# Optimization experiments

Hardware: AMD Instinct MI355X
Metric: run time of the kernel (lower is better)

The kernel has to match this reference:

```python
import jax, jax.numpy as jnp
import numpy as np

MAX_REL = 8  # max_relative_position
B, H, L, D = 2, 16, 2048, 64


def setup_inputs() -> dict:
    key = jax.random.key(0)
    kq, kk, kv, kb = jax.random.split(key, 4)
    return {
        "q": jax.random.normal(kq, (B, H, L, D), dtype=jnp.float32),
        "k": jax.random.normal(kk, (B, H, L, D), dtype=jnp.float32),
        "v": jax.random.normal(kv, (B, H, L, D), dtype=jnp.float32),
        "relative_bias": jax.random.normal(kb, (2 * MAX_REL + 1,), dtype=jnp.float32),
    }


def reference(q, k, v, relative_bias):
    Bq, Hq, Lq, Dq = q.shape
    scale = jnp.sqrt(jnp.asarray(Dq, dtype=q.dtype))
    # [B,H,L,L] attention scores
    scores = jnp.einsum("bhqd,bhkd->bhqk", q, k) / scale
    pos = jnp.arange(Lq)
    rel = pos[None, :] - pos[:, None]                 # [L,L] (col - row), matches torch code
    idx = jnp.clip(rel, -MAX_REL, MAX_REL) + MAX_REL  # [L,L] in [0, 2*MAX_REL]
    bias = relative_bias[idx]                         # [L,L] gather from bias table
    scores = scores + bias[None, None, :, :]
    attn = jax.nn.softmax(scores, axis=-1)
    return jnp.einsum("bhqk,bhkd->bhqd", attn, v)
```

## Files before the change

### kernel.cpp

```cpp
#include <hip/hip_runtime.h>
#include <hip/hip_bf16.h>


#define LOG2E 1.44269504088896f

constexpr int Lv = 2048, Dv = 64;
constexpr int BH  = 32;
constexpr int BQ  = 128;
constexpr int WQ  = 32;
constexpr int BKT = 64;
constexpr int NQT = Lv / BQ;
constexpr int NKT = Lv / BKT;
constexpr int LDK = 72;
constexpr int MAXREL = 8;

typedef __bf16 bf16x8 __attribute__((ext_vector_type(8)));
typedef __bf16 bf16x4 __attribute__((ext_vector_type(4)));
typedef float  f32x4  __attribute__((ext_vector_type(4)));

static __device__ __forceinline__ unsigned pack2bf(float a, float b) {
    __bf16 x = (__bf16)a, y = (__bf16)b;
    unsigned short ux = __builtin_bit_cast(unsigned short, x);
    unsigned short uy = __builtin_bit_cast(unsigned short, y);
    return (unsigned)ux | ((unsigned)uy << 16);
}

__global__ __launch_bounds__(256, 2) void relattn_kernel(
    const float* __restrict__ Q, const float* __restrict__ K,
    const float* __restrict__ V, const float* __restrict__ RB,
    float* __restrict__ O)
{
    __shared__ __align__(16) __bf16 sK[2][BKT * LDK];
    __shared__ __align__(16) __bf16 sV[2][Dv * LDK];
    __shared__ float sRB[2 * MAXREL + 1];

    const int tid  = threadIdx.x;
    const int w    = tid >> 6;
    const int lane = tid & 63;
    const int l16  = lane & 15;
    const int lg   = lane >> 4;

    const int bh = blockIdx.x & (BH - 1);
    const int qt = blockIdx.x >> 5;

    const size_t base = (size_t)bh * Lv * Dv;
    const float* Qb = Q + base + (size_t)qt * BQ * Dv;
    const float* Kb = K + base;
    const float* Vb = V + base;
    float*       Ob = O + base + (size_t)qt * BQ * Dv;

    if (tid < 2 * MAXREL + 1) sRB[tid] = RB[tid] * LOG2E;

    const float qsc = 0.125f * LOG2E;
    bf16x8 qfrag[2][2];
    #pragma unroll
    for (int h = 0; h < 2; ++h) {
        const float* qrow = Qb + (w * WQ + h * 16 + l16) * Dv;
        #pragma unroll
        for (int s = 0; s < 2; ++s) {
            const float4 a = *(const float4*)(qrow + lg * 8 + 32 * s);
            const float4 b = *(const float4*)(qrow + lg * 8 + 32 * s + 4);
            bf16x8 f;
            f[0] = (__bf16)(a.x * qsc); f[1] = (__bf16)(a.y * qsc);
            f[2] = (__bf16)(a.z * qsc); f[3] = (__bf16)(a.w * qsc);
            f[4] = (__bf16)(b.x * qsc); f[5] = (__bf16)(b.y * qsc);
            f[6] = (__bf16)(b.z * qsc); f[7] = (__bf16)(b.w * qsc);
            qfrag[h][s] = f;
        }
    }

    f32x4 oacc[2][4];
    f32x4 lacc[2];
    #pragma unroll
    for (int h = 0; h < 2; ++h) {
        lacc[h] = (f32x4){0.f, 0.f, 0.f, 0.f};
        #pragma unroll
        for (int t = 0; t < 4; ++t)
            #pragma unroll
            for (int r = 0; r < 4; ++r) oacc[h][t][r] = 0.f;
    }

    const int kr0 = tid >> 4;
    const int kc4 = (tid & 15) * 4;
    const int vkk0 = (tid & 31) * 2;
    const int vd0  = (tid >> 5) * 8;
    const int vcol = (vkk0 & 35) | ((vkk0 & 12) << 1) | ((vkk0 & 16) >> 2);

    float4 kreg[4], vreg[4];
    auto loadKV = [&](int kt) {
        const float* Ks = Kb + (size_t)kt * BKT * Dv;
        const float* Vs = Vb + (size_t)kt * BKT * Dv;
        #pragma unroll
        for (int p = 0; p < 4; ++p)
            kreg[p] = *(const float4*)(Ks + (p * 16 + kr0) * Dv + kc4);
        vreg[0] = *(const float4*)(Vs + vkk0 * Dv + vd0);
        vreg[1] = *(const float4*)(Vs + vkk0 * Dv + vd0 + 4);
        vreg[2] = *(const float4*)(Vs + (vkk0 + 1) * Dv + vd0);
        vreg[3] = *(const float4*)(Vs + (vkk0 + 1) * Dv + vd0 + 4);
    };

    loadKV(0);

    const int qw0 = qt * BQ + w * WQ;
    const int qgl = qw0 + l16;

    for (int kt = 0; kt < NKT; ++kt) {
        const int buf = kt & 1;
        #pragma unroll
        for (int p = 0; p < 4; ++p) {
            bf16x4 pk;
            pk[0] = (__bf16)kreg[p].x; pk[1] = (__bf16)kreg[p].y;
            pk[2] = (__bf16)kreg[p].z; pk[3] = (__bf16)kreg[p].w;
            *(bf16x4*)&sK[buf][(p * 16 + kr0) * LDK + kc4] = pk;
        }
        #pragma unroll
        for (int j = 0; j < 4; ++j) {
            *(unsigned*)&sV[buf][(vd0 + j) * LDK + vcol] =
                pack2bf(vreg[0][j], vreg[2][j]);
            *(unsigned*)&sV[buf][(vd0 + 4 + j) * LDK + vcol] =
                pack2bf(vreg[1][j], vreg[3][j]);
        }
        __syncthreads();

        if (kt + 1 < NKT) loadKV(kt + 1);

        f32x4 sacc[2][4];
        #pragma unroll
        for (int h = 0; h < 2; ++h)
            #pragma unroll
            for (int t = 0; t < 4; ++t)
                #pragma unroll
                for (int r = 0; r < 4; ++r) sacc[h][t][r] = 0.f;
        #pragma unroll
        for (int s = 0; s < 2; ++s) {
            #pragma unroll
            for (int t = 0; t < 4; ++t) {
                bf16x8 a = *(const bf16x8*)&sK[buf][(t * 16 + l16) * LDK + lg * 8 + 32 * s];
                sacc[0][t] = __builtin_amdgcn_mfma_f32_16x16x32_bf16(a, qfrag[0][s], sacc[0][t], 0, 0, 0);
                sacc[1][t] = __builtin_amdgcn_mfma_f32_16x16x32_bf16(a, qfrag[1][s], sacc[1][t], 0, 0, 0);
            }
        }

        const int k0 = kt * BKT;
        bf16x8 pfrag[2][2];
        #pragma unroll
        for (int h = 0; h < 2; ++h) {
            const int qw0h = qw0 + h * 16;
            if (k0 >= qw0h + 15 + MAXREL) {
                const float bc = sRB[2 * MAXREL];
                #pragma unroll
                for (int t = 0; t < 4; ++t)
                    #pragma unroll
                    for (int r = 0; r < 4; ++r) {
                        float p = __builtin_amdgcn_exp2f(sacc[h][t][r] + bc);
                        lacc[h][r] += p;
                        pfrag[h][t >> 1][(t & 1) * 4 + r] = (__bf16)p;
                    }
            } else if (k0 + BKT - 1 + MAXREL <= qw0h) {
                const float bc = sRB[0];
                #pragma unroll
                for (int t = 0; t < 4; ++t)
                    #pragma unroll
                    for (int r = 0; r < 4; ++r) {
                        float p = __builtin_amdgcn_exp2f(sacc[h][t][r] + bc);
                        lacc[h][r] += p;
                        pfrag[h][t >> 1][(t & 1) * 4 + r] = (__bf16)p;
                    }
            } else {
                const int kkb = k0 + lg * 4 - (qgl + h * 16);
                #pragma unroll
                for (int t = 0; t < 4; ++t) {
                    #pragma unroll
                    for (int r = 0; r < 4; ++r) {
                        int d = kkb + t * 16 + r;
                        d = d < -MAXREL ? -MAXREL : (d > MAXREL ? MAXREL : d);
                        float p = __builtin_amdgcn_exp2f(sacc[h][t][r] + sRB[d + MAXREL]);
                        lacc[h][r] += p;
                        pfrag[h][t >> 1][(t & 1) * 4 + r] = (__bf16)p;
                    }
                }
            }
        }

        #pragma unroll
        for (int s = 0; s < 2; ++s) {
            #pragma unroll
            for (int t = 0; t < 4; ++t) {
                bf16x8 vf = *(const bf16x8*)&sV[buf][(t * 16 + l16) * LDK + lg * 8 + 32 * s];
                oacc[0][t] = __builtin_amdgcn_mfma_f32_16x16x32_bf16(vf, pfrag[0][s], oacc[0][t], 0, 0, 0);
                oacc[1][t] = __builtin_amdgcn_mfma_f32_16x16x32_bf16(vf, pfrag[1][s], oacc[1][t], 0, 0, 0);
            }
        }
    }

    #pragma unroll
    for (int h = 0; h < 2; ++h) {
        float l = lacc[h][0] + lacc[h][1] + lacc[h][2] + lacc[h][3];
        l += __shfl_xor(l, 16);
        l += __shfl_xor(l, 32);
        const float linv = 1.f / l;
        float* orow = Ob + (w * WQ + h * 16 + l16) * Dv;
        #pragma unroll
        for (int t = 0; t < 4; ++t) {
            float4 o;
            o.x = oacc[h][t][0] * linv; o.y = oacc[h][t][1] * linv;
            o.z = oacc[h][t][2] * linv; o.w = oacc[h][t][3] * linv;
            *(float4*)(orow + t * 16 + lg * 4) = o;
        }
    }
}

extern "C" void kernel_launch(void* const* d_in, const int* in_sizes, int n_in,
                              void* d_out, int out_size, void* d_ws, size_t ws_size,
                              hipStream_t stream) {
    const float* q  = (const float*)d_in[0];
    const float* k  = (const float*)d_in[1];
    const float* v  = (const float*)d_in[2];
    const float* rb = (const float*)d_in[3];
    float* out = (float*)d_out;
    relattn_kernel<<<dim3(BH * NQT), dim3(256), 0, stream>>>(q, k, v, rb, out);
}
```

Baseline: 136.9 us.

## Split key range across two blocks and combine partial outputs in a second kernel

The kernel is templated on a key-split count. With two splits, each block handles half of the key tiles and writes its unnormalized output accumulator and row sum to workspace. A new combine kernel adds the two partials and normalizes. Launch bounds are raised to four blocks per CU, so the doubled grid can fill the device with more concurrent waves. In exchange it writes and re-reads partial results, adds a second launch, tightens the register budget, which risks spills, and only runs when the workspace is large enough.

```diff
diff --git a/kernel.cpp b/kernel.cpp
--- a/kernel.cpp
+++ b/kernel.cpp
@@ -7,7 +7,6 @@
 constexpr int Lv = 2048, Dv = 64;
 constexpr int BH  = 32;
 constexpr int BQ  = 128;
-constexpr int WQ  = 32;
 constexpr int BKT = 64;
 constexpr int NQT = Lv / BQ;
 constexpr int NKT = Lv / BKT;
@@ -25,11 +24,15 @@
     return (unsigned)ux | ((unsigned)uy << 16);
 }
 
-__global__ __launch_bounds__(256, 2) void relattn_kernel(
+template<int NSPLIT>
+__global__ __launch_bounds__(256, 4) void relattn_kernel(
     const float* __restrict__ Q, const float* __restrict__ K,
     const float* __restrict__ V, const float* __restrict__ RB,
-    float* __restrict__ O)
+    float* __restrict__ Out, float* __restrict__ Opart,
+    float* __restrict__ Lpart)
 {
+    constexpr int NI = NKT / NSPLIT;
+
     __shared__ __align__(16) __bf16 sK[2][BKT * LDK];
     __shared__ __align__(16) __bf16 sV[2][Dv * LDK];
     __shared__ float sRB[2 * MAXREL + 1];
@@ -40,14 +43,15 @@
     const int l16  = lane & 15;
     const int lg   = lane >> 4;
 
-    const int bh = blockIdx.x & (BH - 1);
-    const int qt = blockIdx.x >> 5;
+    const int bid = blockIdx.x;
+    const int bh  = bid & (BH - 1);
+    const int qt  = (bid >> 5) & (NQT - 1);
+    const int sp  = bid >> 9;
 
     const size_t base = (size_t)bh * Lv * Dv;
     const float* Qb = Q + base + (size_t)qt * BQ * Dv;
     const float* Kb = K + base;
     const float* Vb = V + base;
-    float*       Ob = O + base + (size_t)qt * BQ * Dv;
 
     if (tid < 2 * MAXREL + 1) sRB[tid] = RB[tid] * LOG2E;
 
@@ -55,7 +59,7 @@
     bf16x8 qfrag[2][2];
     #pragma unroll
     for (int h = 0; h < 2; ++h) {
-        const float* qrow = Qb + (w * WQ + h * 16 + l16) * Dv;
+        const float* qrow = Qb + (w * 32 + h * 16 + l16) * Dv;
         #pragma unroll
         for (int s = 0; s < 2; ++s) {
             const float4 a = *(const float4*)(qrow + lg * 8 + 32 * s);
@@ -99,13 +103,15 @@
         vreg[3] = *(const float4*)(Vs + (vkk0 + 1) * Dv + vd0 + 4);
     };
 
-    loadKV(0);
-
-    const int qw0 = qt * BQ + w * WQ;
+    const int kt0 = sp * NI;
+    loadKV(kt0);
+
+    const int qw0 = qt * BQ + w * 32;
     const int qgl = qw0 + l16;
 
-    for (int kt = 0; kt < NKT; ++kt) {
-        const int buf = kt & 1;
+    for (int i = 0; i < NI; ++i) {
+        const int buf = i & 1;
+        const int kt  = kt0 + i;
         #pragma unroll
         for (int p = 0; p < 4; ++p) {
             bf16x4 pk;
@@ -122,7 +128,7 @@
         }
         __syncthreads();
 
-        if (kt + 1 < NKT) loadKV(kt + 1);
+        if (i + 1 < NI) loadKV(kt + 1);
 
         f32x4 sacc[2][4];
         #pragma unroll
@@ -198,16 +204,41 @@
         float l = lacc[h][0] + lacc[h][1] + lacc[h][2] + lacc[h][3];
         l += __shfl_xor(l, 16);
         l += __shfl_xor(l, 32);
-        const float linv = 1.f / l;
-        float* orow = Ob + (w * WQ + h * 16 + l16) * Dv;
-        #pragma unroll
-        for (int t = 0; t < 4; ++t) {
-            float4 o;
-            o.x = oacc[h][t][0] * linv; o.y = oacc[h][t][1] * linv;
-            o.z = oacc[h][t][2] * linv; o.w = oacc[h][t][3] * linv;
-            *(float4*)(orow + t * 16 + lg * 4) = o;
-        }
-    }
+        const int q = w * 32 + h * 16 + l16;
+        if (NSPLIT == 1) {
+            const float linv = 1.f / l;
+            float* orow = Out + base + (size_t)(qt * BQ + q) * Dv;
+            #pragma unroll
+            for (int t = 0; t < 4; ++t) {
+                float4 o;
+                o.x = oacc[h][t][0] * linv; o.y = oacc[h][t][1] * linv;
+                o.z = oacc[h][t][2] * linv; o.w = oacc[h][t][3] * linv;
+                *(float4*)(orow + t * 16 + lg * 4) = o;
+            }
+        } else {
+            const size_t prow = (size_t)(sp * BH + bh) * Lv + qt * BQ + q;
+            if (lg == 0) Lpart[prow] = l;
+            float* orow = Opart + prow * Dv;
+            #pragma unroll
+            for (int t = 0; t < 4; ++t)
+                *(f32x4*)(orow + t * 16 + lg * 4) = oacc[h][t];
+        }
+    }
+}
+
+__global__ __launch_bounds__(256) void relattn_combine(
+    const float* __restrict__ Opart, const float* __restrict__ Lpart,
+    float* __restrict__ O)
+{
+    const int idx = blockIdx.x * 256 + threadIdx.x;
+    const int row = idx >> 4;
+    const float4 o0 = ((const float4*)Opart)[idx];
+    const float4 o1 = ((const float4*)(Opart + (size_t)BH * Lv * Dv))[idx];
+    const float linv = 1.f / (Lpart[row] + Lpart[row + BH * Lv]);
+    float4 o;
+    o.x = (o0.x + o1.x) * linv; o.y = (o0.y + o1.y) * linv;
+    o.z = (o0.z + o1.z) * linv; o.w = (o0.w + o1.w) * linv;
+    ((float4*)O)[idx] = o;
 }
 
 extern "C" void kernel_launch(void* const* d_in, const int* in_sizes, int n_in,
@@ -218,5 +249,18 @@
     const float* v  = (const float*)d_in[2];
     const float* rb = (const float*)d_in[3];
     float* out = (float*)d_out;
-    relattn_kernel<<<dim3(BH * NQT), dim3(256), 0, stream>>>(q, k, v, rb, out);
-}
+
+    const size_t nO = (size_t)2 * BH * Lv * Dv;
+    const size_t nL = (size_t)2 * BH * Lv;
+    if (ws_size >= (nO + nL) * sizeof(float)) {
+        float* Opart = (float*)d_ws;
+        float* Lpart = Opart + nO;
+        relattn_kernel<2><<<dim3(2 * BH * NQT), dim3(256), 0, stream>>>(
+            q, k, v, rb, out, Opart, Lpart);
+        relattn_combine<<<dim3(BH * Lv * Dv / 4 / 256), dim3(256), 0, stream>>>(
+            Opart, Lpart, out);
+    } else {
+        relattn_kernel<1><<<dim3(BH * NQT), dim3(256), 0, stream>>>(
+            q, k, v, rb, out, nullptr, nullptr);
+    }
+}
```

After: 252.7 us. +84.5%, slower.
